# Optimization experiments

Hardware: AMD Instinct MI355X
Metric: run time of the kernel (lower is better)

Reference implementation:

```python
import jax, jax.numpy as jnp
import numpy as np

FORGET_BIAS = 1.0  # TF BasicLSTMCell default


def setup_inputs() -> dict:
    key = jax.random.key(0)
    ks = jax.random.split(key, 6)
    B, T, D, H, A = 32, 2048, 256, 256, 18
    x = jax.random.normal(ks[0], (B, T, D), dtype=jnp.float32)
    seq_lens = jax.random.randint(ks[1], (B,), 1, T + 1, dtype=jnp.int32)
    c_in = jnp.zeros((B, H), dtype=jnp.float32)
    h_in = jnp.zeros((B, H), dtype=jnp.float32)
    W = jax.random.normal(ks[2], (D + H, 4 * H), dtype=jnp.float32) * 0.05
    b = jnp.zeros((4 * H,), dtype=jnp.float32)
    W_out = jax.random.normal(ks[3], (H, A), dtype=jnp.float32) * 0.01
    b_out = jnp.zeros((A,), dtype=jnp.float32)
    return {"x": x, "seq_lens": seq_lens, "c_in": c_in, "h_in": h_in,
            "W": W, "b": b, "W_out": W_out, "b_out": b_out}


def _lstm_scan(x, seq_lens, c_in, h_in, W, b):
    B, T, D = x.shape
    H = c_in.shape[-1]
    xs = jnp.swapaxes(x, 0, 1)  # [T, B, D] time-major for scan
    ts = jnp.arange(T, dtype=jnp.int32)

    def step(carry, inp):
        c, h = carry
        xt, t = inp
        gates = jnp.concatenate([xt, h], axis=-1) @ W + b  # [B, 4H]
        i, j, f, o = jnp.split(gates, 4, axis=-1)  # TF gate order i, j, f, o
        new_c = c * jax.nn.sigmoid(f + FORGET_BIAS) + jax.nn.sigmoid(i) * jnp.tanh(j)
        new_h = jnp.tanh(new_c) * jax.nn.sigmoid(o)
        mask = (t < seq_lens)[:, None]  # [B, 1]; dynamic_rnn semantics
        c = jnp.where(mask, new_c, c)
        h = jnp.where(mask, new_h, h)
        out = jnp.where(mask, new_h, jnp.zeros_like(new_h))  # zero past length
        return (c, h), out

    (c_fin, h_fin), ys = jax.lax.scan(step, (c_in, h_in), (xs, ts))
    return jnp.swapaxes(ys, 0, 1), c_fin, h_fin  # ys: [B, T, H]


def reference(x, seq_lens, c_in, h_in, W, b, W_out, b_out):
    lstm_out, c_fin, h_fin = _lstm_scan(x, seq_lens, c_in, h_in, W, b)
    H = c_in.shape[-1]
    last_layer = lstm_out.reshape(-1, H)  # [B*T, H]
    logits = last_layer @ W_out + b_out   # [B*T, A]
    return logits, last_layer, c_fin, h_fin
```

## Files before the change

### kernel.cpp

```cpp
#include <hip/hip_runtime.h>
#include <hip/hip_bf16.h>

typedef __attribute__((ext_vector_type(2))) _Float16 half2v;
typedef __attribute__((ext_vector_type(4))) float f32x4;

__device__ __forceinline__ unsigned short f2h_bits(float f) {
    _Float16 h = (_Float16)f;
    return __builtin_bit_cast(unsigned short, h);
}
__device__ __forceinline__ float sigf(float x) { return 1.0f / (1.0f + __expf(-x)); }
__device__ __forceinline__ float tanhf_fast(float x) {
    float ax = fabsf(x);
    float e = __expf(-2.0f * ax);
    float t = (1.0f - e) / (1.0f + e);
    return copysignf(t, x);
}
__device__ __forceinline__ float dot2u(unsigned int w, unsigned int h, float acc) {
    return __builtin_amdgcn_fdot2(__builtin_bit_cast(half2v, w),
                                  __builtin_bit_cast(half2v, h), acc, false);
}
__device__ __forceinline__ float dot2x4(uint4 w, uint4 h, float acc) {
    acc = dot2u(w.x, h.x, acc);
    acc = dot2u(w.y, h.y, acc);
    acc = dot2u(w.z, h.z, acc);
    acc = dot2u(w.w, h.w, acc);
    return acc;
}
__device__ __forceinline__ void pin(uint4& v) {
    asm volatile("" : "+v"(v.x), "+v"(v.y), "+v"(v.z), "+v"(v.w));
}

__global__ void k_flag0(int* __restrict__ prog) { *prog = 0; }

__global__ __launch_bounds__(256) void k_prep(const float* __restrict__ W,
                                              unsigned short* __restrict__ wht) {
    int idx = blockIdx.x * 256 + threadIdx.x;
    int g = idx >> 8, k = idx & 255;
    wht[idx] = f2h_bits(W[(size_t)(256 + k) * 1024 + g]);
}

__global__ __launch_bounds__(256) void k_init(const float* __restrict__ cin,
                                              const float* __restrict__ hin,
                                              float* __restrict__ cc,
                                              float* __restrict__ ch) {
    int i = blockIdx.x * 256 + threadIdx.x;
    cc[i] = cin[i];
    ch[i] = hin[i];
}

__global__ __launch_bounds__(256) void k_gates(const float* __restrict__ x,
                                               const float* __restrict__ W,
                                               const float* __restrict__ bias,
                                               float* __restrict__ gates,
                                               int C, int t0) {
    __shared__ float xs[32][256];
    int tid = threadIdx.x;
    int tc = tid & 31, tr = tid >> 5;
    int r0 = (blockIdx.x >> 3) * 32;
    int c0 = (blockIdx.x & 7) * 128;
    int b  = r0 / C;
    int tl = r0 - b * C;
    const float* xbase = x + ((size_t)b * 2048 + t0 + tl) * 256;

    for (int i = tid; i < 2048; i += 256) {
        int r = i >> 6, kq = (i & 63) << 2;
        *(f32x4*)&xs[r][kq] = *(const f32x4*)(xbase + (size_t)r * 256 + kq);
    }
    __syncthreads();

    f32x4 acc[4];
    f32x4 bb = *(const f32x4*)(bias + c0 + tc * 4);
#pragma unroll
    for (int i = 0; i < 4; ++i) acc[i] = bb;
    const float* wp = W + c0 + tc * 4;
    for (int k = 0; k < 256; k += 2) {
        f32x4 w0 = *(const f32x4*)(wp + (size_t)k * 1024);
        f32x4 w1 = *(const f32x4*)(wp + (size_t)(k + 1) * 1024);
#pragma unroll
        for (int i = 0; i < 4; ++i) {
            float2 xv = *(const float2*)&xs[tr * 4 + i][k];
            acc[i] += w0 * xv.x;
            acc[i] += w1 * xv.y;
        }
    }
#pragma unroll
    for (int i = 0; i < 4; ++i)
        *(f32x4*)(gates + (size_t)(r0 + tr * 4 + i) * 1024 + c0 + tc * 4) = acc[i];
}

__global__ __launch_bounds__(512)
__attribute__((amdgpu_waves_per_eu(2, 2)))
void k_rnn(const unsigned short* __restrict__ wht,
           const float* __restrict__ gates,
           const int* __restrict__ seq_lens,
           float* __restrict__ carry_c,
           float* __restrict__ carry_h,
           int* __restrict__ prog,
           int C, int t0,
           float* __restrict__ out_ll,
           float* __restrict__ out_c,
           float* __restrict__ out_h) {
    extern __shared__ unsigned int smem[];
    uint4* ildsq = (uint4*)smem;
    unsigned short* hs = (unsigned short*)(ildsq + 8192);
    const int tid = threadIdx.x;
    const int u = tid >> 1, p = tid & 1;
    const int w = tid >> 6, l = tid & 63;
    const int b = blockIdx.x;
    if (b == 0 && tid == 0) *prog = 1;

    const uint4* whtq = (const uint4*)wht;
    uint4 wj[16], wf[16], wo[16];
#pragma unroll
    for (int j = 0; j < 16; ++j) {
        wj[j] = whtq[(size_t)(256 + u) * 32 + p * 16 + j];
        wf[j] = whtq[(size_t)(512 + u) * 32 + p * 16 + j];
        wo[j] = whtq[(size_t)(768 + u) * 32 + p * 16 + j];
    }
#pragma unroll
    for (int j = 0; j < 16; ++j) { pin(wj[j]); pin(wf[j]); pin(wo[j]); }
#pragma unroll
    for (int j = 0; j < 16; ++j)
        ildsq[(w * 16 + j) * 64 + l] = whtq[(size_t)u * 32 + p * 16 + j];
    if (b == 0 && tid == 0) *prog = 2;

    float c = carry_c[b * 256 + u];
    float h = carry_h[b * 256 + u];
    if (p == 0) hs[u] = f2h_bits(h);
    int ns = seq_lens[b] - t0;
    ns = ns < 0 ? 0 : (ns > C ? C : ns);
    const float* gxb = gates + (size_t)b * C * 1024;
    float gi = gxb[u], gj = gxb[256 + u], gf = gxb[512 + u], go = gxb[768 + u];
    __syncthreads();

    for (int t = 0; t < ns; ++t) {
        const uint4* hp = (const uint4*)(hs + (t & 1) * 256) + p * 16;
        float ni = 0.f, nj = 0.f, nf = 0.f, no = 0.f;
        if (t + 1 < ns) {
            const float* gn = gxb + (size_t)(t + 1) * 1024;
            ni = gn[u]; nj = gn[256 + u]; nf = gn[512 + u]; no = gn[768 + u];
        }
        float ai = p ? 0.f : gi, aj = p ? 0.f : gj;
        float af = p ? 0.f : gf, ao = p ? 0.f : go;
#pragma unroll
        for (int j = 0; j < 16; ++j) {
            uint4 hv = hp[j];
            uint4 iv = ildsq[(w * 16 + j) * 64 + l];
            ai = dot2x4(iv,    hv, ai);
            aj = dot2x4(wj[j], hv, aj);
            af = dot2x4(wf[j], hv, af);
            ao = dot2x4(wo[j], hv, ao);
        }
        ai += __shfl_xor(ai, 1);
        aj += __shfl_xor(aj, 1);
        af += __shfl_xor(af, 1);
        ao += __shfl_xor(ao, 1);
        if (p == 0) {
            float I = sigf(ai);
            float J = tanhf_fast(aj);
            float F = sigf(af + 1.0f);
            float O = sigf(ao);
            c = c * F + I * J;
            h = tanhf_fast(c) * O;
            out_ll[(size_t)(b * 2048 + t0 + t) * 256 + u] = h;
            hs[((t + 1) & 1) * 256 + u] = f2h_bits(h);
        }
        gi = ni; gj = nj; gf = nf; go = no;
        __syncthreads();
    }
    if (p == 0) {
        carry_c[b * 256 + u] = c;
        carry_h[b * 256 + u] = h;
        out_c[b * 256 + u] = c;
        out_h[b * 256 + u] = h;
    }
    f32x4 z = {0.f, 0.f, 0.f, 0.f};
    f32x4* zp = (f32x4*)(out_ll + (size_t)(b * 2048 + t0 + ns) * 256);
    int cnt = (C - ns) * 64;
    for (int i = tid; i < cnt; i += 512) zp[i] = z;
    if (b == 0 && tid == 0) *prog = 3;
}

__global__ __launch_bounds__(256) void k_logits(const float* __restrict__ ll,
                                                const float* __restrict__ wout,
                                                const float* __restrict__ bout,
                                                float* __restrict__ lg) {
    __shared__ float rows[32][260];
    __shared__ float wo[4608];
    int tid = threadIdx.x;
    size_t r0 = (size_t)blockIdx.x * 32;
    for (int i = tid; i < 4608; i += 256) wo[i] = wout[i];
    const f32x4* src = (const f32x4*)(ll + r0 * 256);
    for (int i = tid; i < 2048; i += 256) {
        int row = i >> 6, c4 = (i & 63) * 4;
        *(f32x4*)&rows[row][c4] = src[i];
    }
    __syncthreads();
    for (int o = tid; o < 576; o += 256) {
        int r = o / 18, a = o - r * 18;
        float acc = bout[a];
#pragma unroll 8
        for (int k = 0; k < 256; ++k)
            acc += rows[r][k] * wo[k * 18 + a];
        lg[(r0 + r) * 18 + a] = acc;
    }
}

__global__ __launch_bounds__(256) void k_diag(const float* __restrict__ gates,
                                              const int* __restrict__ prog,
                                              int wsb, int nsample,
                                              float* __restrict__ logit0) {
    __shared__ float red[256];
    int tid = threadIdx.x;
    float m = 0.f; int bad_nan = 0;
    for (int i = tid; i < nsample; i += 256) {
        float v = gates[i];
        if (v != v) bad_nan = 1;
        m = fmaxf(m, fabsf(v));
    }
    red[tid] = bad_nan ? 3.0e38f : m;
    __syncthreads();
    for (int s = 128; s > 0; s >>= 1) {
        if (tid < s) red[tid] = fmaxf(red[tid], red[tid + s]);
        __syncthreads();
    }
    if (tid == 0) {
        float l = log2f(1.0f + red[0]);
        int R = *prog; R = R < 0 ? 0 : (R > 3 ? 3 : R);
        int G = (int)(l * 0.5f); G = G < 0 ? 0 : (G > 7 ? 7 : G);
        int good = (R == 3) && (l <= 4.0f) && (wsb >= 1);
        if (!good) {
            int code = (R << 5) | (G << 2) | wsb;
            *logit0 = (float)(256 + 2 * code);
        }
    }
}

extern "C" void kernel_launch(void* const* d_in, const int* in_sizes, int n_in,
                              void* d_out, int out_size, void* d_ws, size_t ws_size,
                              hipStream_t stream) {
    const float* x = nullptr; const int* seq = nullptr;
    const float* cin = nullptr, *hin = nullptr, *W = nullptr, *bia = nullptr,
               * Wo = nullptr, *bo = nullptr;
    int n8192 = 0;
    for (int i = 0; i < n_in; ++i) {
        switch (in_sizes[i]) {
            case 16777216: x   = (const float*)d_in[i]; break;
            case 32:       seq = (const int*)d_in[i];   break;
            case 524288:   W   = (const float*)d_in[i]; break;
            case 1024:     bia = (const float*)d_in[i]; break;
            case 4608:     Wo  = (const float*)d_in[i]; break;
            case 18:       bo  = (const float*)d_in[i]; break;
            case 8192:
                if (n8192 == 0) cin = (const float*)d_in[i];
                else if (n8192 == 1) hin = (const float*)d_in[i];
                ++n8192; break;
        }
    }
    if (!x)   x   = (const float*)d_in[0];
    if (!seq) seq = (const int*)d_in[1];
    if (!cin) cin = (const float*)d_in[2];
    if (!hin) hin = (const float*)d_in[3];
    if (!W)   W   = (const float*)d_in[4];
    if (!bia) bia = (const float*)d_in[5];
    if (!Wo)  Wo  = (const float*)d_in[6];
    if (!bo)  bo  = (const float*)d_in[7];

    unsigned short* wht = (unsigned short*)d_ws;
    float* carry_c = (float*)((char*)d_ws + 524288);
    float* carry_h = (float*)((char*)d_ws + 557056);
    int*   prog    = (int*)((char*)d_ws + 589824);
    float* gates   = (float*)((char*)d_ws + 593920);
    const size_t fixed = 593920;

    int wsb;
    if (ws_size < fixed + (size_t)64 * 131072) wsb = 0;
    else if (ws_size < ((size_t)70 << 20))  wsb = 1;
    else if (ws_size < ((size_t)280 << 20)) wsb = 2;
    else wsb = 3;

    int C = 2048;
    while (C > 64 && fixed + (size_t)C * 131072 > ws_size) C >>= 1;
    int NC = 2048 / C;

    float* out = (float*)d_out;
    float* o_logits = out;
    float* o_ll = out + 1179648;
    float* o_c  = out + 17956864;
    float* o_h  = out + 17965056;

    (void)hipFuncSetAttribute(reinterpret_cast<const void*>(&k_rnn),
                              hipFuncAttributeMaxDynamicSharedMemorySize, 132096);

    hipLaunchKernelGGL(k_flag0, dim3(1), dim3(1), 0, stream, prog);
    int nsample = 0;
    if (wsb >= 1) {
        hipLaunchKernelGGL(k_prep, dim3(1024), dim3(256), 0, stream, W, wht);
        hipLaunchKernelGGL(k_init, dim3(32),   dim3(256), 0, stream, cin, hin,
                           carry_c, carry_h);
        for (int ch = 0; ch < NC; ++ch) {
            int t0 = ch * C;
            hipLaunchKernelGGL(k_gates, dim3(8 * C), dim3(256), 0, stream,
                               x, W, bia, gates, C, t0);
            hipLaunchKernelGGL(k_rnn, dim3(32), dim3(512), 132096, stream,
                               wht, gates, seq, carry_c, carry_h, prog, C, t0,
                               o_ll, o_c, o_h);
        }
        nsample = 4096;
    }
    hipLaunchKernelGGL(k_logits, dim3(2048), dim3(256), 0, stream, o_ll, Wo, bo, o_logits);
    hipLaunchKernelGGL(k_diag, dim3(1), dim3(256), 0, stream,
                       gates, prog, wsb, nsample, o_logits);
}
```

Baseline: 4.710 ms.

## Rebalance LSTM recurrent weights between registers and LDS, reduce pairs with DPP

The recurrent weight matrix is repacked so that each thread's slice is contiguous. More of the weights now live in LDS (18 chunks per wave instead of 16), which cuts the per-thread register array to relieve VGPR pressure. The pair reduction now uses a DPP swap instead of shfl_xor. Because the larger weight block fills the LDS allocation, the double-buffered h state moves to a per-block global-memory buffer. That adds global-memory latency to every step of the serial recurrence.

```diff
diff --git a/kernel.cpp b/kernel.cpp
--- a/kernel.cpp
+++ b/kernel.cpp
@@ -29,14 +29,25 @@
 __device__ __forceinline__ void pin(uint4& v) {
     asm volatile("" : "+v"(v.x), "+v"(v.y), "+v"(v.z), "+v"(v.w));
 }
+__device__ __forceinline__ float pair_sum(float a) {
+    int y = __builtin_amdgcn_update_dpp(0, __builtin_bit_cast(int, a),
+                                        0xB1, 0xF, 0xF, true);
+    return a + __builtin_bit_cast(float, y);
+}
 
 __global__ void k_flag0(int* __restrict__ prog) { *prog = 0; }
 
 __global__ __launch_bounds__(256) void k_prep(const float* __restrict__ W,
                                               unsigned short* __restrict__ wht) {
     int idx = blockIdx.x * 256 + threadIdx.x;
-    int g = idx >> 8, k = idx & 255;
-    wht[idx] = f2h_bits(W[(size_t)(256 + k) * 1024 + g]);
+    int e = idx & 7;
+    int j = (idx >> 3) & 15;
+    int g = (idx >> 7) & 3;
+    int p = (idx >> 9) & 1;
+    int u = idx >> 10;
+    int k   = p * 128 + j * 8 + e;
+    int col = g * 256 + u;
+    wht[idx] = f2h_bits(W[(size_t)(256 + k) * 1024 + col]);
 }
 
 __global__ __launch_bounds__(256) void k_init(const float* __restrict__ cin,
@@ -95,6 +106,7 @@
            const int* __restrict__ seq_lens,
            float* __restrict__ carry_c,
            float* __restrict__ carry_h,
+           unsigned short* __restrict__ hg,
            int* __restrict__ prog,
            int C, int t0,
            float* __restrict__ out_ll,
@@ -102,70 +114,102 @@
            float* __restrict__ out_h) {
     extern __shared__ unsigned int smem[];
     uint4* ildsq = (uint4*)smem;
-    unsigned short* hs = (unsigned short*)(ildsq + 8192);
     const int tid = threadIdx.x;
-    const int u = tid >> 1, p = tid & 1;
     const int w = tid >> 6, l = tid & 63;
+    const int u = tid >> 1;
+    const int p = tid & 1;
     const int b = blockIdx.x;
     if (b == 0 && tid == 0) *prog = 1;
 
     const uint4* whtq = (const uint4*)wht;
-    uint4 wj[16], wf[16], wo[16];
-#pragma unroll
-    for (int j = 0; j < 16; ++j) {
-        wj[j] = whtq[(size_t)(256 + u) * 32 + p * 16 + j];
-        wf[j] = whtq[(size_t)(512 + u) * 32 + p * 16 + j];
-        wo[j] = whtq[(size_t)(768 + u) * 32 + p * 16 + j];
-    }
-#pragma unroll
-    for (int j = 0; j < 16; ++j) { pin(wj[j]); pin(wf[j]); pin(wo[j]); }
-#pragma unroll
-    for (int j = 0; j < 16; ++j)
-        ildsq[(w * 16 + j) * 64 + l] = whtq[(size_t)u * 32 + p * 16 + j];
+    const uint4* wbase = whtq + (size_t)tid * 64;
+
+    uint4 w1[14], w2[16], w3[16];
+#pragma unroll
+    for (int j = 0; j < 14; ++j) w1[j] = wbase[1 * 16 + 2 + j];
+#pragma unroll
+    for (int j = 0; j < 16; ++j) w2[j] = wbase[2 * 16 + j];
+#pragma unroll
+    for (int j = 0; j < 16; ++j) w3[j] = wbase[3 * 16 + j];
+
+#pragma unroll
+    for (int jj = 0; jj < 16; ++jj)
+        ildsq[(w * 18 + jj) * 64 + l] = wbase[0 * 16 + jj];
+#pragma unroll
+    for (int jj = 0; jj < 2; ++jj)
+        ildsq[(w * 18 + 16 + jj) * 64 + l] = wbase[1 * 16 + jj];
     if (b == 0 && tid == 0) *prog = 2;
 
-    float c = carry_c[b * 256 + u];
-    float h = carry_h[b * 256 + u];
-    if (p == 0) hs[u] = f2h_bits(h);
+    unsigned short* hgb = hg + (size_t)b * 512;
+    float c = 0.f, h = 0.f;
     int ns = seq_lens[b] - t0;
     ns = ns < 0 ? 0 : (ns > C ? C : ns);
     const float* gxb = gates + (size_t)b * C * 1024;
-    float gi = gxb[u], gj = gxb[256 + u], gf = gxb[512 + u], go = gxb[768 + u];
+    float pg0 = 0.f, pg1 = 0.f, pg2 = 0.f, pg3 = 0.f;
+    if (p == 0) {
+        c = carry_c[b * 256 + u];
+        h = carry_h[b * 256 + u];
+        hgb[u] = f2h_bits(h);
+        if (ns > 0) {
+            pg0 = gxb[u];       pg1 = gxb[256 + u];
+            pg2 = gxb[512 + u]; pg3 = gxb[768 + u];
+        }
+    }
     __syncthreads();
 
     for (int t = 0; t < ns; ++t) {
-        const uint4* hp = (const uint4*)(hs + (t & 1) * 256) + p * 16;
-        float ni = 0.f, nj = 0.f, nf = 0.f, no = 0.f;
-        if (t + 1 < ns) {
+#pragma unroll
+        for (int j = 0; j < 14; ++j) pin(w1[j]);
+#pragma unroll
+        for (int j = 0; j < 16; ++j) pin(w2[j]);
+#pragma unroll
+        for (int j = 0; j < 16; ++j) pin(w3[j]);
+
+        float ng0 = 0.f, ng1 = 0.f, ng2 = 0.f, ng3 = 0.f;
+        if (t + 1 < ns && p == 0) {
             const float* gn = gxb + (size_t)(t + 1) * 1024;
-            ni = gn[u]; nj = gn[256 + u]; nf = gn[512 + u]; no = gn[768 + u];
-        }
-        float ai = p ? 0.f : gi, aj = p ? 0.f : gj;
-        float af = p ? 0.f : gf, ao = p ? 0.f : go;
-#pragma unroll
-        for (int j = 0; j < 16; ++j) {
-            uint4 hv = hp[j];
-            uint4 iv = ildsq[(w * 16 + j) * 64 + l];
-            ai = dot2x4(iv,    hv, ai);
-            aj = dot2x4(wj[j], hv, aj);
-            af = dot2x4(wf[j], hv, af);
-            ao = dot2x4(wo[j], hv, ao);
-        }
-        ai += __shfl_xor(ai, 1);
-        aj += __shfl_xor(aj, 1);
-        af += __shfl_xor(af, 1);
-        ao += __shfl_xor(ao, 1);
+            ng0 = gn[u];       ng1 = gn[256 + u];
+            ng2 = gn[512 + u]; ng3 = gn[768 + u];
+        }
+
+        float a0 = (p == 0) ? pg0 : 0.f;
+        float a1 = (p == 0) ? pg1 : 0.f;
+        float a2 = (p == 0) ? pg2 : 0.f;
+        float a3 = (p == 0) ? pg3 : 0.f;
+
+        const uint4* hvp = (const uint4*)(hgb + (t & 1) * 256 + p * 128);
+#pragma unroll
+        for (int ck = 0; ck < 4; ++ck) {
+            uint4 hvr[4];
+#pragma unroll
+            for (int jc = 0; jc < 4; ++jc) hvr[jc] = hvp[ck * 4 + jc];
+#pragma unroll
+            for (int jc = 0; jc < 4; ++jc) {
+                const int j = ck * 4 + jc;
+                a0 = dot2x4(ildsq[(w * 18 + j) * 64 + l], hvr[jc], a0);
+                if (j < 2)
+                    a1 = dot2x4(ildsq[(w * 18 + 16 + j) * 64 + l], hvr[jc], a1);
+                else
+                    a1 = dot2x4(w1[j - 2], hvr[jc], a1);
+                a2 = dot2x4(w2[j], hvr[jc], a2);
+                a3 = dot2x4(w3[j], hvr[jc], a3);
+            }
+        }
+        a0 = pair_sum(a0);
+        a1 = pair_sum(a1);
+        a2 = pair_sum(a2);
+        a3 = pair_sum(a3);
         if (p == 0) {
-            float I = sigf(ai);
-            float J = tanhf_fast(aj);
-            float F = sigf(af + 1.0f);
-            float O = sigf(ao);
+            float I = sigf(a0);
+            float J = tanhf_fast(a1);
+            float F = sigf(a2 + 1.0f);
+            float O = sigf(a3);
             c = c * F + I * J;
             h = tanhf_fast(c) * O;
             out_ll[(size_t)(b * 2048 + t0 + t) * 256 + u] = h;
-            hs[((t + 1) & 1) * 256 + u] = f2h_bits(h);
-        }
-        gi = ni; gj = nj; gf = nf; go = no;
+            hgb[((t + 1) & 1) * 256 + u] = f2h_bits(h);
+        }
+        pg0 = ng0; pg1 = ng1; pg2 = ng2; pg3 = ng3;
         __syncthreads();
     }
     if (p == 0) {
@@ -270,8 +314,9 @@
     float* carry_c = (float*)((char*)d_ws + 524288);
     float* carry_h = (float*)((char*)d_ws + 557056);
     int*   prog    = (int*)((char*)d_ws + 589824);
-    float* gates   = (float*)((char*)d_ws + 593920);
-    const size_t fixed = 593920;
+    unsigned short* hg = (unsigned short*)((char*)d_ws + 593920);
+    float* gates   = (float*)((char*)d_ws + 626688);
+    const size_t fixed = 626688;
 
     int wsb;
     if (ws_size < fixed + (size_t)64 * 131072) wsb = 0;
@@ -290,7 +335,7 @@
     float* o_h  = out + 17965056;
 
     (void)hipFuncSetAttribute(reinterpret_cast<const void*>(&k_rnn),
-                              hipFuncAttributeMaxDynamicSharedMemorySize, 132096);
+                              hipFuncAttributeMaxDynamicSharedMemorySize, 147456);
 
     hipLaunchKernelGGL(k_flag0, dim3(1), dim3(1), 0, stream, prog);
     int nsample = 0;
@@ -302,8 +347,8 @@
             int t0 = ch * C;
             hipLaunchKernelGGL(k_gates, dim3(8 * C), dim3(256), 0, stream,
                                x, W, bia, gates, C, t0);
-            hipLaunchKernelGGL(k_rnn, dim3(32), dim3(512), 132096, stream,
-                               wht, gates, seq, carry_c, carry_h, prog, C, t0,
+            hipLaunchKernelGGL(k_rnn, dim3(32), dim3(512), 147456, stream,
+                               wht, gates, seq, carry_c, carry_h, hg, prog, C, t0,
                                o_ll, o_c, o_h);
         }
         nsample = 4096;
```

Result: slower. 6.091 ms (+29.3%).

## Split each batch row's recurrence across four blocks synchronized via global atomics

Applied to the files above, without the earlier changes.

Each batch element's LSTM recurrence now runs on four workgroups instead of one. Each block owns 64 hidden units across all four gates, keeps its weight slice in registers, and drops the LDS-resident gate weights. Hidden state is exchanged each step through a global fp16 buffer, with atomic counters and spin-waits acting as a cross-block barrier. This cuts per-step dot-product work per block and raises occupancy to 128 blocks. In exchange it adds a global-memory round trip and spin latency every timestep, and depends on all four blocks being co-resident (there is a timeout bail-out).

```diff
diff --git a/kernel.cpp b/kernel.cpp
--- a/kernel.cpp
+++ b/kernel.cpp
@@ -35,17 +35,26 @@
 __global__ __launch_bounds__(256) void k_prep(const float* __restrict__ W,
                                               unsigned short* __restrict__ wht) {
     int idx = blockIdx.x * 256 + threadIdx.x;
-    int g = idx >> 8, k = idx & 255;
-    wht[idx] = f2h_bits(W[(size_t)(256 + k) * 1024 + g]);
+    int gcol = idx >> 8;
+    int k    = idx & 255;
+    wht[idx] = f2h_bits(W[(size_t)(256 + k) * 1024 + gcol]);
 }
 
 __global__ __launch_bounds__(256) void k_init(const float* __restrict__ cin,
                                               const float* __restrict__ hin,
                                               float* __restrict__ cc,
-                                              float* __restrict__ ch) {
+                                              float* __restrict__ ch,
+                                              unsigned short* __restrict__ hg,
+                                              int* __restrict__ prog) {
     int i = blockIdx.x * 256 + threadIdx.x;
     cc[i] = cin[i];
     ch[i] = hin[i];
+    hg[(i >> 8) * 512 + (i & 255)] = f2h_bits(hin[i]);
+    if (threadIdx.x == 0) {
+        int* line = (int*)((char*)prog + 64 + blockIdx.x * 64);
+        line[0] = 0;
+        line[8] = 0;
+    }
 }
 
 __global__ __launch_bounds__(256) void k_gates(const float* __restrict__ x,
@@ -89,96 +98,149 @@
 }
 
 __global__ __launch_bounds__(512)
-__attribute__((amdgpu_waves_per_eu(2, 2)))
 void k_rnn(const unsigned short* __restrict__ wht,
            const float* __restrict__ gates,
            const int* __restrict__ seq_lens,
            float* __restrict__ carry_c,
            float* __restrict__ carry_h,
+           unsigned short* __restrict__ hg,
            int* __restrict__ prog,
            int C, int t0,
            float* __restrict__ out_ll,
            float* __restrict__ out_c,
            float* __restrict__ out_h) {
-    extern __shared__ unsigned int smem[];
-    uint4* ildsq = (uint4*)smem;
-    unsigned short* hs = (unsigned short*)(ildsq + 8192);
+    __shared__ unsigned short hs[512];
+    __shared__ float part[512];
+    __shared__ int bail;
     const int tid = threadIdx.x;
-    const int u = tid >> 1, p = tid & 1;
-    const int w = tid >> 6, l = tid & 63;
-    const int b = blockIdx.x;
-    if (b == 0 && tid == 0) *prog = 1;
-
-    const uint4* whtq = (const uint4*)wht;
-    uint4 wj[16], wf[16], wo[16];
-#pragma unroll
-    for (int j = 0; j < 16; ++j) {
-        wj[j] = whtq[(size_t)(256 + u) * 32 + p * 16 + j];
-        wf[j] = whtq[(size_t)(512 + u) * 32 + p * 16 + j];
-        wo[j] = whtq[(size_t)(768 + u) * 32 + p * 16 + j];
-    }
-#pragma unroll
-    for (int j = 0; j < 16; ++j) { pin(wj[j]); pin(wf[j]); pin(wo[j]); }
-#pragma unroll
-    for (int j = 0; j < 16; ++j)
-        ildsq[(w * 16 + j) * 64 + l] = whtq[(size_t)u * 32 + p * 16 + j];
-    if (b == 0 && tid == 0) *prog = 2;
-
-    float c = carry_c[b * 256 + u];
-    float h = carry_h[b * 256 + u];
-    if (p == 0) hs[u] = f2h_bits(h);
+    const int w = tid >> 6;
+    const int slot = blockIdx.x;
+    const int xcd = slot & 7, idx = slot >> 3;
+    const int b = xcd * 4 + (idx & 3);
+    const int g = idx >> 2;
+    const int U0 = g * 64;
+    const int col = tid & 255;
+    const int p   = tid >> 8;
+    const int gate = col >> 6, uu = col & 63;
+    const int gcol = gate * 256 + U0 + uu;
+    if (tid == 0) bail = 0;
+    if (slot == 0 && tid == 0) *prog = 1;
+
+    const uint4* wbase = (const uint4*)wht + ((size_t)gcol * 2 + p) * 16;
+    uint4 wr[16];
+#pragma unroll
+    for (int j = 0; j < 16; ++j) wr[j] = wbase[j];
+
     int ns = seq_lens[b] - t0;
     ns = ns < 0 ? 0 : (ns > C ? C : ns);
     const float* gxb = gates + (size_t)b * C * 1024;
-    float gi = gxb[u], gj = gxb[256 + u], gf = gxb[512 + u], go = gxb[768 + u];
+    unsigned short* hgb = hg + (size_t)b * 512;
+    int* cnt  = (int*)((char*)prog + 64 + b * 64);
+    int* pres = cnt + 8;
+
+    if (tid == 0) {
+        __hip_atomic_fetch_add(pres, 1, __ATOMIC_RELEASE, __HIP_MEMORY_SCOPE_AGENT);
+        const int ptarget = 4 * (t0 / C + 1);
+        int spins = 0;
+        while (__hip_atomic_load(pres, __ATOMIC_ACQUIRE,
+                                 __HIP_MEMORY_SCOPE_AGENT) < ptarget) {
+            __builtin_amdgcn_s_sleep(1);
+            if (++spins > (1 << 20)) { bail = 1; *prog = 7; break; }
+        }
+    }
+    __syncthreads();
+    if (bail) { if (slot == 0 && tid == 0) *prog = 7; return; }
+    if (slot == 0 && tid == 0) *prog = 2;
+
+    float c = 0.f, hl = 0.f;
+    if (tid < 64) {
+        c  = carry_c[b * 256 + U0 + tid];
+        hl = carry_h[b * 256 + U0 + tid];
+    }
+    if (tid < 32)
+        *((uint4*)hs + (t0 & 1) * 32 + tid) = *((const uint4*)hgb + (t0 & 1) * 32 + tid);
+    float pg = 0.f;
+    if (p == 0 && ns > 0) pg = gxb[gcol];
     __syncthreads();
 
     for (int t = 0; t < ns; ++t) {
-        const uint4* hp = (const uint4*)(hs + (t & 1) * 256) + p * 16;
-        float ni = 0.f, nj = 0.f, nf = 0.f, no = 0.f;
-        if (t + 1 < ns) {
-            const float* gn = gxb + (size_t)(t + 1) * 1024;
-            ni = gn[u]; nj = gn[256 + u]; nf = gn[512 + u]; no = gn[768 + u];
-        }
-        float ai = p ? 0.f : gi, aj = p ? 0.f : gj;
-        float af = p ? 0.f : gf, ao = p ? 0.f : go;
-#pragma unroll
-        for (int j = 0; j < 16; ++j) {
-            uint4 hv = hp[j];
-            uint4 iv = ildsq[(w * 16 + j) * 64 + l];
-            ai = dot2x4(iv,    hv, ai);
-            aj = dot2x4(wj[j], hv, aj);
-            af = dot2x4(wf[j], hv, af);
-            ao = dot2x4(wo[j], hv, ao);
-        }
-        ai += __shfl_xor(ai, 1);
-        aj += __shfl_xor(aj, 1);
-        af += __shfl_xor(af, 1);
-        ao += __shfl_xor(ao, 1);
-        if (p == 0) {
+        const int pr = (t0 + t) & 1;
+#pragma unroll
+        for (int j = 0; j < 16; ++j) pin(wr[j]);
+
+        float ng = 0.f;
+        if (p == 0 && t + 1 < ns)
+            ng = gxb[(size_t)(t + 1) * 1024 + gcol];
+
+        const uint4* hq = (const uint4*)hs + pr * 32 + p * 16;
+        float a0 = (p == 0) ? pg : 0.f, a1 = 0.f, a2 = 0.f, a3 = 0.f;
+#pragma unroll
+        for (int j = 0; j < 16; j += 4) {
+            uint4 h0 = hq[j], h1 = hq[j + 1], h2 = hq[j + 2], h3 = hq[j + 3];
+            a0 = dot2x4(wr[j],     h0, a0);
+            a1 = dot2x4(wr[j + 1], h1, a1);
+            a2 = dot2x4(wr[j + 2], h2, a2);
+            a3 = dot2x4(wr[j + 3], h3, a3);
+        }
+        part[p * 256 + col] = (a0 + a1) + (a2 + a3);
+        __syncthreads();
+
+        if (tid < 64) {
+            float ai = part[tid]       + part[256 + tid];
+            float aj = part[64 + tid]  + part[320 + tid];
+            float af = part[128 + tid] + part[384 + tid];
+            float ao = part[192 + tid] + part[448 + tid];
             float I = sigf(ai);
             float J = tanhf_fast(aj);
             float F = sigf(af + 1.0f);
             float O = sigf(ao);
             c = c * F + I * J;
-            h = tanhf_fast(c) * O;
-            out_ll[(size_t)(b * 2048 + t0 + t) * 256 + u] = h;
-            hs[((t + 1) & 1) * 256 + u] = f2h_bits(h);
-        }
-        gi = ni; gj = nj; gf = nf; go = no;
+            float hn = tanhf_fast(c) * O;
+            hl = hn;
+            out_ll[(size_t)(b * 2048 + t0 + t) * 256 + U0 + tid] = hn;
+            hgb[(pr ^ 1) * 256 + U0 + tid] = f2h_bits(hn);
+        }
+        if (w == 0) {
+            __threadfence();
+            if (tid == 0)
+                __hip_atomic_fetch_add(cnt, 1, __ATOMIC_RELEASE,
+                                       __HIP_MEMORY_SCOPE_AGENT);
+        }
+        if (t + 1 < ns) {
+            if (tid == 0) {
+                const int target = 4 * (t0 + t + 1);
+                int spins = 0;
+                while (__hip_atomic_load(cnt, __ATOMIC_ACQUIRE,
+                                         __HIP_MEMORY_SCOPE_AGENT) < target) {
+                    __builtin_amdgcn_s_sleep(1);
+                    if (++spins > (1 << 20)) { bail = 1; *prog = 7; break; }
+                }
+            }
+            __syncthreads();
+            if (bail) break;
+            if (tid < 32) {
+                __threadfence();
+                *((uint4*)hs + (pr ^ 1) * 32 + tid) =
+                    *((const uint4*)hgb + (pr ^ 1) * 32 + tid);
+            }
+        }
+        pg = ng;
         __syncthreads();
     }
-    if (p == 0) {
-        carry_c[b * 256 + u] = c;
-        carry_h[b * 256 + u] = h;
-        out_c[b * 256 + u] = c;
-        out_h[b * 256 + u] = h;
+
+    if (tid < 64) {
+        carry_c[b * 256 + U0 + tid] = c;
+        carry_h[b * 256 + U0 + tid] = hl;
+        out_c[b * 256 + U0 + tid] = c;
+        out_h[b * 256 + U0 + tid] = hl;
     }
     f32x4 z = {0.f, 0.f, 0.f, 0.f};
-    f32x4* zp = (f32x4*)(out_ll + (size_t)(b * 2048 + t0 + ns) * 256);
-    int cnt = (C - ns) * 64;
-    for (int i = tid; i < cnt; i += 512) zp[i] = z;
-    if (b == 0 && tid == 0) *prog = 3;
+    int cnt4 = (C - ns) * 16;
+    for (int i = tid; i < cnt4; i += 512) {
+        int r = i >> 4, q4 = i & 15;
+        *(f32x4*)(out_ll + (size_t)(b * 2048 + t0 + ns + r) * 256 + U0 + q4 * 4) = z;
+    }
+    if (slot == 0 && tid == 0 && !bail) *prog = 3;
 }
 
 __global__ __launch_bounds__(256) void k_logits(const float* __restrict__ ll,
@@ -226,7 +288,7 @@
     }
     if (tid == 0) {
         float l = log2f(1.0f + red[0]);
-        int R = *prog; R = R < 0 ? 0 : (R > 3 ? 3 : R);
+        int R = *prog; R = R < 0 ? 0 : (R > 7 ? 7 : R);
         int G = (int)(l * 0.5f); G = G < 0 ? 0 : (G > 7 ? 7 : G);
         int good = (R == 3) && (l <= 4.0f) && (wsb >= 1);
         if (!good) {
@@ -270,8 +332,9 @@
     float* carry_c = (float*)((char*)d_ws + 524288);
     float* carry_h = (float*)((char*)d_ws + 557056);
     int*   prog    = (int*)((char*)d_ws + 589824);
-    float* gates   = (float*)((char*)d_ws + 593920);
-    const size_t fixed = 593920;
+    unsigned short* hg = (unsigned short*)((char*)d_ws + 593920);
+    float* gates   = (float*)((char*)d_ws + 626688);
+    const size_t fixed = 626688;
 
     int wsb;
     if (ws_size < fixed + (size_t)64 * 131072) wsb = 0;
@@ -289,21 +352,18 @@
     float* o_c  = out + 17956864;
     float* o_h  = out + 17965056;
 
-    (void)hipFuncSetAttribute(reinterpret_cast<const void*>(&k_rnn),
-                              hipFuncAttributeMaxDynamicSharedMemorySize, 132096);
-
     hipLaunchKernelGGL(k_flag0, dim3(1), dim3(1), 0, stream, prog);
     int nsample = 0;
     if (wsb >= 1) {
         hipLaunchKernelGGL(k_prep, dim3(1024), dim3(256), 0, stream, W, wht);
         hipLaunchKernelGGL(k_init, dim3(32),   dim3(256), 0, stream, cin, hin,
-                           carry_c, carry_h);
+                           carry_c, carry_h, hg, prog);
         for (int ch = 0; ch < NC; ++ch) {
             int t0 = ch * C;
             hipLaunchKernelGGL(k_gates, dim3(8 * C), dim3(256), 0, stream,
                                x, W, bia, gates, C, t0);
-            hipLaunchKernelGGL(k_rnn, dim3(32), dim3(512), 132096, stream,
-                               wht, gates, seq, carry_c, carry_h, prog, C, t0,
+            hipLaunchKernelGGL(k_rnn, dim3(128), dim3(512), 0, stream,
+                               wht, gates, seq, carry_c, carry_h, hg, prog, C, t0,
                                o_ll, o_c, o_h);
         }
         nsample = 4096;
```

New measurement: 10.52 ms. 123% more time.
